# Optimization experiments

Measured on AMD Instinct MI355X. Metric: run time of the kernel, lower is better.

The kernel has to match this reference:

```python
import jax, jax.numpy as jnp
import numpy as np

B = 65536
H = W = 28
K = 3
OUT_HW = H - K + 1  # 26, valid conv
FEAT = OUT_HW * OUT_HW  # 676
HID = 200
NCLS = 10


def setup_inputs() -> dict:
    key = jax.random.key(0)
    ks = jax.random.split(key, 6)
    x = jax.random.normal(ks[0], (B, H * W), dtype=jnp.float32)
    conv_w = jnp.ones((K, K), dtype=jnp.float32)  # Parameter(ones((3,3)))
    w1 = jax.random.normal(ks[1], (FEAT, HID), dtype=jnp.float32) * (1.0 / np.sqrt(FEAT))
    b1 = jnp.zeros((HID,), dtype=jnp.float32)
    w2 = jax.random.normal(ks[2], (HID, NCLS), dtype=jnp.float32) * (1.0 / np.sqrt(HID))
    b2 = jnp.zeros((NCLS,), dtype=jnp.float32)
    return {"x": x, "conv_w": conv_w, "w1": w1, "b1": b1, "w2": w2, "b2": b2}


def _forward(x, conv_w, w1, b1, w2, b2):
    img = x.reshape(-1, H, W)  # (B,28,28)
    # valid 3x3 single-channel cross-correlation (matches input[i:i+3,j:j+3]*w)
    lhs = img[:, None, :, :]          # (B,1,28,28)
    rhs = conv_w[None, None, :, :]    # (1,1,3,3)
    conv = jax.lax.conv_general_dilated(
        lhs, rhs, window_strides=(1, 1), padding="VALID",
        dimension_numbers=("NCHW", "OIHW", "NCHW"))  # (B,1,26,26)
    feat = conv.reshape(-1, FEAT)     # (B,676)
    hidden = jax.nn.relu(feat @ w1 + b1)  # (B,200)
    return hidden @ w2 + b2               # (B,10) logits


def reference(x, conv_w, w1, b1, w2, b2):
    return _forward(x, conv_w, w1, b1, w2, b2)
```

## Files before the change

kernel.cpp:

```cpp
#include <hip/hip_runtime.h>
#include <hip/hip_bf16.h>

#define BATCH   65536
#define HW      28
#define OHW     26
#define FEAT    676
#define HID     200
#define NCLS    10
#define MT2     64
#define GBLOCKS (BATCH / MT2)
#define KC1     25

typedef __attribute__((ext_vector_type(8))) __bf16 bf16x8;
typedef __attribute__((ext_vector_type(4))) float  f32x4;

#define KBAR() asm volatile("s_waitcnt lgkmcnt(0)\n\ts_barrier" ::: "memory")

__device__ __forceinline__ unsigned int pk2(float a, float b) {
  __hip_bfloat16 ha = __float2bfloat16(a), hb = __float2bfloat16(b);
  return (unsigned int)__builtin_bit_cast(unsigned short, ha)
       | ((unsigned int)__builtin_bit_cast(unsigned short, hb) << 16);
}

__device__ __forceinline__ unsigned short* fslot(unsigned short* base, int m, int k) {
  const int kc = k >> 5;
  return base + ((kc * 64 + ((k >> 3) & 3) * 16 + (m ^ (kc & 7))) * 8) + (k & 7);
}

__global__ __launch_bounds__(256) void prep_w1e(const float* __restrict__ w1,
                                                const float* __restrict__ cwp,
                                                unsigned short* __restrict__ w1e) {
  int c = blockIdx.x * 256 + threadIdx.x;
  if (c >= KC1 * 13 * 64) return;
  int lane = c & 63, g = c >> 6;
  int kc = g / 13, nt = g - kc * 13;
  int ln = lane & 15, qd = lane >> 4;
  int n = nt * 16 + ln;
  float cw[9];
  #pragma unroll
  for (int t = 0; t < 9; ++t) cw[t] = cwp[t];
  float v[8];
  #pragma unroll
  for (int j = 0; j < 8; ++j) {
    int k = kc * 32 + qd * 8 + j;
    float s = 0.f;
    if (k < 784 && n < HID) {
      int ri = k / 28, ci = k - ri * 28;
      #pragma unroll
      for (int di = 0; di < 3; ++di) {
        int r = ri - di;
        if (r >= 0 && r < OHW) {
          #pragma unroll
          for (int dj = 0; dj < 3; ++dj) {
            int cc = ci - dj;
            if (cc >= 0 && cc < OHW) s += cw[di * 3 + dj] * w1[(r * OHW + cc) * HID + n];
          }
        }
      }
    }
    v[j] = s;
  }
  uint4 o = make_uint4(pk2(v[0], v[1]), pk2(v[2], v[3]),
                       pk2(v[4], v[5]), pk2(v[6], v[7]));
  *(uint4*)(w1e + (size_t)c * 8) = o;
}

__global__ __launch_bounds__(256) void prep_w2f(const float* __restrict__ w2,
                                                unsigned short* __restrict__ w2f) {
  int c = blockIdx.x * 256 + threadIdx.x;
  if (c >= 7 * 64) return;
  int lane = c & 63, kc = c >> 6;
  int col = lane & 15;
  float v[8];
  #pragma unroll
  for (int j = 0; j < 8; ++j) {
    int k = kc * 32 + (lane >> 4) * 8 + j;
    v[j] = (col < NCLS && k < HID) ? w2[k * NCLS + col] : 0.f;
  }
  uint4 o = make_uint4(pk2(v[0], v[1]), pk2(v[2], v[3]),
                       pk2(v[4], v[5]), pk2(v[6], v[7]));
  *(uint4*)(w2f + (size_t)c * 8) = o;
}

template<int NT0, int NT>
__device__ __forceinline__ void gemm1_body(
    const float* __restrict__ x, const unsigned short* __restrict__ w1e,
    const float* __restrict__ b1, unsigned short* aBuf ,
    unsigned short* hidA, int lane, int tid, int blk64) {
  const int ln = lane & 15, qd = lane >> 4;

  const int sc_mi  = tid >> 6;
  const int sc_qd  = (tid >> 4) & 3;
  const int sc_row = tid & 15;
  const float* xrow = x + ((size_t)blk64 + sc_mi * 16 + sc_row) * 784 + sc_qd * 8;
  const int sc_off = (sc_mi * 64 + sc_qd * 16 + sc_row) * 8;

  f32x4 acc[4][NT];
  #pragma unroll
  for (int mi = 0; mi < 4; ++mi)
    #pragma unroll
    for (int t = 0; t < NT; ++t) acc[mi][t] = (f32x4){0.f, 0.f, 0.f, 0.f};

  {
    float4 f0 = *(const float4*)(xrow);
    float4 f1 = *(const float4*)(xrow + 4);
    *(uint4*)(aBuf + sc_off) = make_uint4(pk2(f0.x, f0.y), pk2(f0.z, f0.w),
                                          pk2(f1.x, f1.y), pk2(f1.z, f1.w));
  }
  __syncthreads();

  int cur = 0;
  for (int kc = 0; kc < KC1; ++kc) {
    uint4 nx;
    const bool hav = (kc + 1 < KC1);
    if (hav) {
      if (kc + 1 == KC1 - 1 && sc_qd >= 2) {
        nx = make_uint4(0u, 0u, 0u, 0u);
      } else {
        float4 f0 = *(const float4*)(xrow + (kc + 1) * 32);
        float4 f1 = *(const float4*)(xrow + (kc + 1) * 32 + 4);
        nx = make_uint4(pk2(f0.x, f0.y), pk2(f0.z, f0.w),
                        pk2(f1.x, f1.y), pk2(f1.z, f1.w));
      }
    }
    const unsigned short* ab = aBuf + cur * 2048;
    bf16x8 a[4];
    #pragma unroll
    for (int mi = 0; mi < 4; ++mi)
      a[mi] = *(const bf16x8*)(ab + mi * 512 + lane * 8);
    #pragma unroll
    for (int t = 0; t < NT; ++t) {
      bf16x8 b = *(const bf16x8*)(w1e + ((size_t)(kc * 13 + NT0 + t) * 64 + lane) * 8);
      #pragma unroll
      for (int mi = 0; mi < 4; ++mi)
        acc[mi][t] = __builtin_amdgcn_mfma_f32_16x16x32_bf16(a[mi], b, acc[mi][t], 0, 0, 0);
    }
    if (hav) *(uint4*)(aBuf + (cur ^ 1) * 2048 + sc_off) = nx;
    KBAR();
    cur ^= 1;
  }

  #pragma unroll
  for (int t = 0; t < NT; ++t) {
    const int n = (NT0 + t) * 16 + ln;
    if (n < HID) {
      const float bias = b1[n];
      const int kc2 = n >> 5, qd2 = (n >> 3) & 3, j2 = n & 7, c2 = kc2 & 7;
      #pragma unroll
      for (int mi = 0; mi < 4; ++mi)
        #pragma unroll
        for (int rr = 0; rr < 4; ++rr) {
          const int m = qd * 4 + rr;
          float h = fmaxf(acc[mi][t][rr] + bias, 0.f);
          __hip_bfloat16 hb = __float2bfloat16(h);
          hidA[mi * 3584 + (kc2 * 64 + qd2 * 16 + (m ^ c2)) * 8 + j2] =
              __builtin_bit_cast(unsigned short, hb);
        }
    }
  }
}

__global__ __launch_bounds__(256, 4) void fused6(
    const float* __restrict__ x, const unsigned short* __restrict__ w1e,
    const unsigned short* __restrict__ w2f, const float* __restrict__ b1,
    const float* __restrict__ b2, float* __restrict__ out) {
  __shared__ __align__(16) unsigned short aBuf[2 * 4 * 64 * 8];
  __shared__ __align__(16) unsigned short hidA[4 * 7 * 64 * 8];
  const int tid  = threadIdx.x;
  const int wave = tid >> 6;
  const int lane = tid & 63;
  const int blk64 = blockIdx.x * MT2;

  for (int i = tid; i < 768; i += 256) {
    int mi = i / 192, r = i - mi * 192, m = r / 12, d = r - m * 12;
    *(unsigned int*)fslot(hidA + mi * 3584, m, 200 + 2 * d) = 0u;
  }

  switch (wave) {
    case 0:  gemm1_body<0, 4>(x, w1e, b1, aBuf, hidA, lane, tid, blk64); break;
    case 1:  gemm1_body<4, 3>(x, w1e, b1, aBuf, hidA, lane, tid, blk64); break;
    case 2:  gemm1_body<7, 3>(x, w1e, b1, aBuf, hidA, lane, tid, blk64); break;
    default: gemm1_body<10, 3>(x, w1e, b1, aBuf, hidA, lane, tid, blk64); break;
  }
  __syncthreads();

  const int ln = lane & 15, qd = lane >> 4;
  f32x4 acc2 = (f32x4){0.f, 0.f, 0.f, 0.f};
  #pragma unroll
  for (int kc = 0; kc < 7; ++kc) {
    bf16x8 a = *(const bf16x8*)&hidA[wave * 3584 + (kc * 64 + (lane ^ (kc & 7))) * 8];
    bf16x8 b = *(const bf16x8*)(w2f + ((size_t)kc * 64 + lane) * 8);
    acc2 = __builtin_amdgcn_mfma_f32_16x16x32_bf16(a, b, acc2, 0, 0, 0);
  }
  if (ln < NCLS) {
    const float bb = b2[ln];
    #pragma unroll
    for (int rr = 0; rr < 4; ++rr) {
      out[((size_t)(blockIdx.x * 4 + wave) * 16 + qd * 4 + rr) * NCLS + ln] = acc2[rr] + bb;
    }
  }
}

extern "C" void kernel_launch(void* const* d_in, const int* in_sizes, int n_in,
                              void* d_out, int out_size, void* d_ws, size_t ws_size,
                              hipStream_t stream) {
  const float* x  = (const float*)d_in[0];
  const float* cw = (const float*)d_in[1];
  const float* w1 = (const float*)d_in[2];
  const float* b1 = (const float*)d_in[3];
  const float* w2 = (const float*)d_in[4];
  const float* b2 = (const float*)d_in[5];
  float* out = (float*)d_out;

  unsigned short* w1e = (unsigned short*)d_ws;
  unsigned short* w2f = (unsigned short*)((char*)d_ws + 335872);

  hipLaunchKernelGGL(prep_w1e, dim3((KC1 * 13 * 64 + 255) / 256), dim3(256), 0, stream,
                     w1, cw, w1e);
  hipLaunchKernelGGL(prep_w2f, dim3(2), dim3(256), 0, stream, w2, w2f);
  hipLaunchKernelGGL(fused6, dim3(GBLOCKS), dim3(256), 0, stream,
                     x, w1e, w2f, b1, b2, out);
}
```

Baseline: 320.9 us.

## Stage W1 tiles through LDS with double buffering and triple-buffer the x tiles

Each block now cooperatively loads the per-k-chunk W1 fragments into a double-buffered LDS region instead of having each wave read them from global memory on every use. The x activation tiles move to a triple buffer so loads run two chunks ahead, and the hidden-activation buffer reuses the same shared region after the GEMM1 loop. The aim is to cut redundant global/L2 traffic for weights and hide load latency. In exchange each thread holds more in-flight registers and the block uses more LDS (about 38 KB), which could limit occupancy.

```diff
diff --git a/kernel.cpp b/kernel.cpp
--- a/kernel.cpp
+++ b/kernel.cpp
@@ -10,6 +10,11 @@
 #define MT2     64
 #define GBLOCKS (BATCH / MT2)
 #define KC1     25
+
+#define ABUF    2048
+#define BOFF    6144
+#define BBUF    6656
+#define SHTOT   19456
 
 typedef __attribute__((ext_vector_type(8))) __bf16 bf16x8;
 typedef __attribute__((ext_vector_type(4))) float  f32x4;
@@ -85,15 +90,13 @@
 template<int NT0, int NT>
 __device__ __forceinline__ void gemm1_body(
     const float* __restrict__ x, const unsigned short* __restrict__ w1e,
-    const float* __restrict__ b1, unsigned short* aBuf ,
-    unsigned short* hidA, int lane, int tid, int blk64) {
+    const float* __restrict__ b1, unsigned short* sh,
+    int lane, int tid, int blk64) {
   const int ln = lane & 15, qd = lane >> 4;
 
-  const int sc_mi  = tid >> 6;
-  const int sc_qd  = (tid >> 4) & 3;
-  const int sc_row = tid & 15;
-  const float* xrow = x + ((size_t)blk64 + sc_mi * 16 + sc_row) * 784 + sc_qd * 8;
-  const int sc_off = (sc_mi * 64 + sc_qd * 16 + sc_row) * 8;
+  const int sc_qd = (tid >> 4) & 3;
+  const float* xrow = x + ((size_t)blk64 + (tid >> 6) * 16 + (tid & 15)) * 784 + sc_qd * 8;
+  const int t3ok = (tid + 768) < 832;
 
   f32x4 acc[4][NT];
   #pragma unroll
@@ -104,40 +107,79 @@
   {
     float4 f0 = *(const float4*)(xrow);
     float4 f1 = *(const float4*)(xrow + 4);
-    *(uint4*)(aBuf + sc_off) = make_uint4(pk2(f0.x, f0.y), pk2(f0.z, f0.w),
-                                          pk2(f1.x, f1.y), pk2(f1.z, f1.w));
+    float4 g0 = *(const float4*)(xrow + 32);
+    float4 g1 = *(const float4*)(xrow + 36);
+    *(uint4*)(sh + tid * 8) = make_uint4(pk2(f0.x, f0.y), pk2(f0.z, f0.w),
+                                         pk2(f1.x, f1.y), pk2(f1.z, f1.w));
+    *(uint4*)(sh + ABUF + tid * 8) = make_uint4(pk2(g0.x, g0.y), pk2(g0.z, g0.w),
+                                                pk2(g1.x, g1.y), pk2(g1.z, g1.w));
+    uint4 b0 = *(const uint4*)(w1e + (size_t)tid * 8);
+    uint4 b1v = *(const uint4*)(w1e + (size_t)(tid + 256) * 8);
+    uint4 b2v = *(const uint4*)(w1e + (size_t)(tid + 512) * 8);
+    *(uint4*)(sh + BOFF + tid * 8) = b0;
+    *(uint4*)(sh + BOFF + (tid + 256) * 8) = b1v;
+    *(uint4*)(sh + BOFF + (tid + 512) * 8) = b2v;
+    if (t3ok) {
+      uint4 b3v = *(const uint4*)(w1e + (size_t)(tid + 768) * 8);
+      *(uint4*)(sh + BOFF + (tid + 768) * 8) = b3v;
+    }
   }
   __syncthreads();
 
-  int cur = 0;
   for (int kc = 0; kc < KC1; ++kc) {
-    uint4 nx;
-    const bool hav = (kc + 1 < KC1);
-    if (hav) {
-      if (kc + 1 == KC1 - 1 && sc_qd >= 2) {
-        nx = make_uint4(0u, 0u, 0u, 0u);
-      } else {
-        float4 f0 = *(const float4*)(xrow + (kc + 1) * 32);
-        float4 f1 = *(const float4*)(xrow + (kc + 1) * 32 + 4);
-        nx = make_uint4(pk2(f0.x, f0.y), pk2(f0.z, f0.w),
-                        pk2(f1.x, f1.y), pk2(f1.z, f1.w));
-      }
-    }
-    const unsigned short* ab = aBuf + cur * 2048;
+    uint4 bq0, bq1, bq2, bq3;
+    const bool havB = (kc + 1 < KC1);
+    if (havB) {
+      const unsigned short* wsrc = w1e + (size_t)(kc + 1) * 832 * 8;
+      bq0 = *(const uint4*)(wsrc + (size_t)tid * 8);
+      bq1 = *(const uint4*)(wsrc + (size_t)(tid + 256) * 8);
+      bq2 = *(const uint4*)(wsrc + (size_t)(tid + 512) * 8);
+      if (t3ok) bq3 = *(const uint4*)(wsrc + (size_t)(tid + 768) * 8);
+    }
+    float4 fq0, fq1;
+    const bool havA = (kc + 2 < KC1);
+    const bool atail = (kc + 2 == KC1 - 1) && (sc_qd >= 2);
+    if (havA && !atail) {
+      fq0 = *(const float4*)(xrow + (kc + 2) * 32);
+      fq1 = *(const float4*)(xrow + (kc + 2) * 32 + 4);
+    }
+
+    const unsigned short* ab = sh + (kc % 3) * ABUF;
+    const unsigned short* bb = sh + BOFF + (kc & 1) * BBUF;
     bf16x8 a[4];
     #pragma unroll
     for (int mi = 0; mi < 4; ++mi)
       a[mi] = *(const bf16x8*)(ab + mi * 512 + lane * 8);
     #pragma unroll
     for (int t = 0; t < NT; ++t) {
-      bf16x8 b = *(const bf16x8*)(w1e + ((size_t)(kc * 13 + NT0 + t) * 64 + lane) * 8);
+      bf16x8 b = *(const bf16x8*)(bb + ((NT0 + t) * 64 + lane) * 8);
       #pragma unroll
       for (int mi = 0; mi < 4; ++mi)
         acc[mi][t] = __builtin_amdgcn_mfma_f32_16x16x32_bf16(a[mi], b, acc[mi][t], 0, 0, 0);
     }
-    if (hav) *(uint4*)(aBuf + (cur ^ 1) * 2048 + sc_off) = nx;
+
+    if (havA) {
+      uint4 cv;
+      if (atail) cv = make_uint4(0u, 0u, 0u, 0u);
+      else       cv = make_uint4(pk2(fq0.x, fq0.y), pk2(fq0.z, fq0.w),
+                                 pk2(fq1.x, fq1.y), pk2(fq1.z, fq1.w));
+      *(uint4*)(sh + ((kc + 2) % 3) * ABUF + tid * 8) = cv;
+    }
+    if (havB) {
+      unsigned short* bdst = sh + BOFF + ((kc + 1) & 1) * BBUF;
+      *(uint4*)(bdst + tid * 8) = bq0;
+      *(uint4*)(bdst + (tid + 256) * 8) = bq1;
+      *(uint4*)(bdst + (tid + 512) * 8) = bq2;
+      if (t3ok) *(uint4*)(bdst + (tid + 768) * 8) = bq3;
+    }
     KBAR();
-    cur ^= 1;
+  }
+
+  __syncthreads();
+
+  for (int i = tid; i < 768; i += 256) {
+    int mi = i / 192, r = i - mi * 192, m = r / 12, d = r - m * 12;
+    *(unsigned int*)fslot(sh + mi * 3584, m, 200 + 2 * d) = 0u;
   }
 
   #pragma unroll
@@ -153,34 +195,28 @@
           const int m = qd * 4 + rr;
           float h = fmaxf(acc[mi][t][rr] + bias, 0.f);
           __hip_bfloat16 hb = __float2bfloat16(h);
-          hidA[mi * 3584 + (kc2 * 64 + qd2 * 16 + (m ^ c2)) * 8 + j2] =
+          sh[mi * 3584 + (kc2 * 64 + qd2 * 16 + (m ^ c2)) * 8 + j2] =
               __builtin_bit_cast(unsigned short, hb);
         }
     }
   }
 }
 
-__global__ __launch_bounds__(256, 4) void fused6(
+__global__ __launch_bounds__(256, 4) void fused7(
     const float* __restrict__ x, const unsigned short* __restrict__ w1e,
     const unsigned short* __restrict__ w2f, const float* __restrict__ b1,
     const float* __restrict__ b2, float* __restrict__ out) {
-  __shared__ __align__(16) unsigned short aBuf[2 * 4 * 64 * 8];
-  __shared__ __align__(16) unsigned short hidA[4 * 7 * 64 * 8];
+  __shared__ __align__(16) unsigned short sh[SHTOT];
   const int tid  = threadIdx.x;
   const int wave = tid >> 6;
   const int lane = tid & 63;
   const int blk64 = blockIdx.x * MT2;
 
-  for (int i = tid; i < 768; i += 256) {
-    int mi = i / 192, r = i - mi * 192, m = r / 12, d = r - m * 12;
-    *(unsigned int*)fslot(hidA + mi * 3584, m, 200 + 2 * d) = 0u;
-  }
-
   switch (wave) {
-    case 0:  gemm1_body<0, 4>(x, w1e, b1, aBuf, hidA, lane, tid, blk64); break;
-    case 1:  gemm1_body<4, 3>(x, w1e, b1, aBuf, hidA, lane, tid, blk64); break;
-    case 2:  gemm1_body<7, 3>(x, w1e, b1, aBuf, hidA, lane, tid, blk64); break;
-    default: gemm1_body<10, 3>(x, w1e, b1, aBuf, hidA, lane, tid, blk64); break;
+    case 0:  gemm1_body<0, 4>(x, w1e, b1, sh, lane, tid, blk64); break;
+    case 1:  gemm1_body<4, 3>(x, w1e, b1, sh, lane, tid, blk64); break;
+    case 2:  gemm1_body<7, 3>(x, w1e, b1, sh, lane, tid, blk64); break;
+    default: gemm1_body<10, 3>(x, w1e, b1, sh, lane, tid, blk64); break;
   }
   __syncthreads();
 
@@ -188,7 +224,7 @@
   f32x4 acc2 = (f32x4){0.f, 0.f, 0.f, 0.f};
   #pragma unroll
   for (int kc = 0; kc < 7; ++kc) {
-    bf16x8 a = *(const bf16x8*)&hidA[wave * 3584 + (kc * 64 + (lane ^ (kc & 7))) * 8];
+    bf16x8 a = *(const bf16x8*)&sh[wave * 3584 + (kc * 64 + (lane ^ (kc & 7))) * 8];
     bf16x8 b = *(const bf16x8*)(w2f + ((size_t)kc * 64 + lane) * 8);
     acc2 = __builtin_amdgcn_mfma_f32_16x16x32_bf16(a, b, acc2, 0, 0, 0);
   }
@@ -218,6 +254,6 @@
   hipLaunchKernelGGL(prep_w1e, dim3((KC1 * 13 * 64 + 255) / 256), dim3(256), 0, stream,
                      w1, cw, w1e);
   hipLaunchKernelGGL(prep_w2f, dim3(2), dim3(256), 0, stream, w2, w2f);
-  hipLaunchKernelGGL(fused6, dim3(GBLOCKS), dim3(256), 0, stream,
+  hipLaunchKernelGGL(fused7, dim3(GBLOCKS), dim3(256), 0, stream,
                      x, w1e, w2f, b1, b2, out);
 }
```

New measurement: 323.6 us. No clear change (+0.8%).

## Deepen x prefetch to distance two and register-prefetch W1 fragments

Applied to the files above, without the earlier changes.

The GEMM1 K-loop now loads x rows two chunks ahead into registers and also prefetches the next chunk's W1 B-fragments into registers, so global loads overlap with the MFMAs instead of being issued just before use. The loop is fully unrolled and the staging offset is simplified to tid*8. Launch bounds drop from 4 to 3 blocks per CU to make room for the extra registers. The cost is higher register pressure and lower occupancy.

```diff
diff --git a/kernel.cpp b/kernel.cpp
--- a/kernel.cpp
+++ b/kernel.cpp
@@ -20,6 +20,11 @@
   __hip_bfloat16 ha = __float2bfloat16(a), hb = __float2bfloat16(b);
   return (unsigned int)__builtin_bit_cast(unsigned short, ha)
        | ((unsigned int)__builtin_bit_cast(unsigned short, hb) << 16);
+}
+
+__device__ __forceinline__ uint4 pk8(float4 f0, float4 f1) {
+  return make_uint4(pk2(f0.x, f0.y), pk2(f0.z, f0.w),
+                    pk2(f1.x, f1.y), pk2(f1.z, f1.w));
 }
 
 __device__ __forceinline__ unsigned short* fslot(unsigned short* base, int m, int k) {
@@ -89,11 +94,9 @@
     unsigned short* hidA, int lane, int tid, int blk64) {
   const int ln = lane & 15, qd = lane >> 4;
 
-  const int sc_mi  = tid >> 6;
-  const int sc_qd  = (tid >> 4) & 3;
-  const int sc_row = tid & 15;
-  const float* xrow = x + ((size_t)blk64 + sc_mi * 16 + sc_row) * 784 + sc_qd * 8;
-  const int sc_off = (sc_mi * 64 + sc_qd * 16 + sc_row) * 8;
+  const int sc_qd = (tid >> 4) & 3;
+  const float* xrow =
+      x + ((size_t)blk64 + (tid >> 6) * 16 + (tid & 15)) * 784 + sc_qd * 8;
 
   f32x4 acc[4][NT];
   #pragma unroll
@@ -102,42 +105,57 @@
     for (int t = 0; t < NT; ++t) acc[mi][t] = (f32x4){0.f, 0.f, 0.f, 0.f};
 
   {
-    float4 f0 = *(const float4*)(xrow);
-    float4 f1 = *(const float4*)(xrow + 4);
-    *(uint4*)(aBuf + sc_off) = make_uint4(pk2(f0.x, f0.y), pk2(f0.z, f0.w),
-                                          pk2(f1.x, f1.y), pk2(f1.z, f1.w));
-  }
+    float4 p0 = *(const float4*)(xrow);
+    float4 p1 = *(const float4*)(xrow + 4);
+    *(uint4*)(aBuf + tid * 8) = pk8(p0, p1);
+  }
+  float4 a1l0 = *(const float4*)(xrow + 32), a1l1 = *(const float4*)(xrow + 36);
+  float4 a2l0 = *(const float4*)(xrow + 64), a2l1 = *(const float4*)(xrow + 68);
+  bf16x8 bCur[NT];
+  #pragma unroll
+  for (int t = 0; t < NT; ++t)
+    bCur[t] = *(const bf16x8*)(w1e + ((size_t)((NT0 + t) * 64 + lane)) * 8);
   __syncthreads();
 
-  int cur = 0;
+  #pragma unroll
   for (int kc = 0; kc < KC1; ++kc) {
-    uint4 nx;
-    const bool hav = (kc + 1 < KC1);
-    if (hav) {
-      if (kc + 1 == KC1 - 1 && sc_qd >= 2) {
-        nx = make_uint4(0u, 0u, 0u, 0u);
+    if (kc + 1 < KC1)
+      *(uint4*)(aBuf + ((kc + 1) & 1) * 2048 + tid * 8) = pk8(a1l0, a1l1);
+    a1l0 = a2l0; a1l1 = a2l1;
+
+    bf16x8 bNx[NT];
+    if (kc + 1 < KC1) {
+      #pragma unroll
+      for (int t = 0; t < NT; ++t)
+        bNx[t] = *(const bf16x8*)(w1e +
+                   ((size_t)((kc + 1) * 13 + NT0 + t) * 64 + lane) * 8);
+    }
+    if (kc + 3 < KC1) {
+      if (kc + 3 == KC1 - 1 && sc_qd >= 2) {
+        a2l0 = (float4){0.f, 0.f, 0.f, 0.f};
+        a2l1 = (float4){0.f, 0.f, 0.f, 0.f};
       } else {
-        float4 f0 = *(const float4*)(xrow + (kc + 1) * 32);
-        float4 f1 = *(const float4*)(xrow + (kc + 1) * 32 + 4);
-        nx = make_uint4(pk2(f0.x, f0.y), pk2(f0.z, f0.w),
-                        pk2(f1.x, f1.y), pk2(f1.z, f1.w));
+        a2l0 = *(const float4*)(xrow + (kc + 3) * 32);
+        a2l1 = *(const float4*)(xrow + (kc + 3) * 32 + 4);
       }
     }
-    const unsigned short* ab = aBuf + cur * 2048;
+
+    const unsigned short* ab = aBuf + (kc & 1) * 2048;
     bf16x8 a[4];
     #pragma unroll
     for (int mi = 0; mi < 4; ++mi)
       a[mi] = *(const bf16x8*)(ab + mi * 512 + lane * 8);
     #pragma unroll
-    for (int t = 0; t < NT; ++t) {
-      bf16x8 b = *(const bf16x8*)(w1e + ((size_t)(kc * 13 + NT0 + t) * 64 + lane) * 8);
+    for (int t = 0; t < NT; ++t)
       #pragma unroll
       for (int mi = 0; mi < 4; ++mi)
-        acc[mi][t] = __builtin_amdgcn_mfma_f32_16x16x32_bf16(a[mi], b, acc[mi][t], 0, 0, 0);
-    }
-    if (hav) *(uint4*)(aBuf + (cur ^ 1) * 2048 + sc_off) = nx;
+        acc[mi][t] = __builtin_amdgcn_mfma_f32_16x16x32_bf16(a[mi], bCur[t],
+                                                             acc[mi][t], 0, 0, 0);
+    if (kc + 1 < KC1) {
+      #pragma unroll
+      for (int t = 0; t < NT; ++t) bCur[t] = bNx[t];
+    }
     KBAR();
-    cur ^= 1;
   }
 
   #pragma unroll
@@ -160,11 +178,11 @@
   }
 }
 
-__global__ __launch_bounds__(256, 4) void fused6(
+__global__ __launch_bounds__(256, 3) void fused8(
     const float* __restrict__ x, const unsigned short* __restrict__ w1e,
     const unsigned short* __restrict__ w2f, const float* __restrict__ b1,
     const float* __restrict__ b2, float* __restrict__ out) {
-  __shared__ __align__(16) unsigned short aBuf[2 * 4 * 64 * 8];
+  __shared__ __align__(16) unsigned short aBuf[2 * 2048];
   __shared__ __align__(16) unsigned short hidA[4 * 7 * 64 * 8];
   const int tid  = threadIdx.x;
   const int wave = tid >> 6;
@@ -218,6 +236,6 @@
   hipLaunchKernelGGL(prep_w1e, dim3((KC1 * 13 * 64 + 255) / 256), dim3(256), 0, stream,
                      w1, cw, w1e);
   hipLaunchKernelGGL(prep_w2f, dim3(2), dim3(256), 0, stream, w2, w2f);
-  hipLaunchKernelGGL(fused6, dim3(GBLOCKS), dim3(256), 0, stream,
+  hipLaunchKernelGGL(fused8, dim3(GBLOCKS), dim3(256), 0, stream,
                      x, w1e, w2f, b1, b2, out);
 }
```

Measured after the change: 328.0 us. 1.02x slower.

## Process two K-chunks per barrier, share LDS for hidden, merge prep kernels

Applied to the files above, without the earlier changes.

The GEMM1 loop now stages 64 K-elements per iteration (two 32-wide chunks) into a double buffer, halving the number of barriers and making each prefetch larger. The staging buffer and hidden-activation buffer are merged into one shared array, with the epilogue moved after a barrier, which reduces LDS per block and may help occupancy. The two weight-prep kernels are merged into one launch. The loop is fully unrolled, which raises register pressure and can cost spills.

```diff
diff --git a/kernel.cpp b/kernel.cpp
--- a/kernel.cpp
+++ b/kernel.cpp
@@ -4,12 +4,12 @@
 #define BATCH   65536
 #define HW      28
 #define OHW     26
-#define FEAT    676
 #define HID     200
 #define NCLS    10
 #define MT2     64
 #define GBLOCKS (BATCH / MT2)
-#define KC1     25
+#define KC32    26
+#define NSTEP   13
 
 typedef __attribute__((ext_vector_type(8))) __bf16 bf16x8;
 typedef __attribute__((ext_vector_type(4))) float  f32x4;
@@ -22,124 +22,151 @@
        | ((unsigned int)__builtin_bit_cast(unsigned short, hb) << 16);
 }
 
+__device__ __forceinline__ uint4 pk8(float4 f0, float4 f1) {
+  return make_uint4(pk2(f0.x, f0.y), pk2(f0.z, f0.w),
+                    pk2(f1.x, f1.y), pk2(f1.z, f1.w));
+}
+
 __device__ __forceinline__ unsigned short* fslot(unsigned short* base, int m, int k) {
   const int kc = k >> 5;
   return base + ((kc * 64 + ((k >> 3) & 3) * 16 + (m ^ (kc & 7))) * 8) + (k & 7);
 }
 
-__global__ __launch_bounds__(256) void prep_w1e(const float* __restrict__ w1,
-                                                const float* __restrict__ cwp,
-                                                unsigned short* __restrict__ w1e) {
-  int c = blockIdx.x * 256 + threadIdx.x;
-  if (c >= KC1 * 13 * 64) return;
-  int lane = c & 63, g = c >> 6;
-  int kc = g / 13, nt = g - kc * 13;
-  int ln = lane & 15, qd = lane >> 4;
-  int n = nt * 16 + ln;
-  float cw[9];
-  #pragma unroll
-  for (int t = 0; t < 9; ++t) cw[t] = cwp[t];
-  float v[8];
-  #pragma unroll
-  for (int j = 0; j < 8; ++j) {
-    int k = kc * 32 + qd * 8 + j;
-    float s = 0.f;
-    if (k < 784 && n < HID) {
-      int ri = k / 28, ci = k - ri * 28;
-      #pragma unroll
-      for (int di = 0; di < 3; ++di) {
-        int r = ri - di;
-        if (r >= 0 && r < OHW) {
-          #pragma unroll
-          for (int dj = 0; dj < 3; ++dj) {
-            int cc = ci - dj;
-            if (cc >= 0 && cc < OHW) s += cw[di * 3 + dj] * w1[(r * OHW + cc) * HID + n];
+__global__ __launch_bounds__(256) void prep_weights(
+    const float* __restrict__ w1, const float* __restrict__ cwp,
+    const float* __restrict__ w2, unsigned short* __restrict__ w1e,
+    unsigned short* __restrict__ w2f) {
+  if (blockIdx.x < 85) {
+    int c = blockIdx.x * 256 + threadIdx.x;
+    if (c >= KC32 * 13 * 64) return;
+    int lane = c & 63, g = c >> 6;
+    int kc = g / 13, nt = g - kc * 13;
+    int ln = lane & 15, qd = lane >> 4;
+    int n = nt * 16 + ln;
+    float cw[9];
+    #pragma unroll
+    for (int t = 0; t < 9; ++t) cw[t] = cwp[t];
+    float v[8];
+    #pragma unroll
+    for (int j = 0; j < 8; ++j) {
+      int k = kc * 32 + qd * 8 + j;
+      float s = 0.f;
+      if (k < 784 && n < HID) {
+        int ri = k / 28, ci = k - ri * 28;
+        #pragma unroll
+        for (int di = 0; di < 3; ++di) {
+          int r = ri - di;
+          if (r >= 0 && r < OHW) {
+            #pragma unroll
+            for (int dj = 0; dj < 3; ++dj) {
+              int cc = ci - dj;
+              if (cc >= 0 && cc < OHW)
+                s += cw[di * 3 + dj] * w1[(r * OHW + cc) * HID + n];
+            }
           }
         }
       }
-    }
-    v[j] = s;
-  }
-  uint4 o = make_uint4(pk2(v[0], v[1]), pk2(v[2], v[3]),
-                       pk2(v[4], v[5]), pk2(v[6], v[7]));
-  *(uint4*)(w1e + (size_t)c * 8) = o;
-}
-
-__global__ __launch_bounds__(256) void prep_w2f(const float* __restrict__ w2,
-                                                unsigned short* __restrict__ w2f) {
-  int c = blockIdx.x * 256 + threadIdx.x;
-  if (c >= 7 * 64) return;
-  int lane = c & 63, kc = c >> 6;
-  int col = lane & 15;
-  float v[8];
-  #pragma unroll
-  for (int j = 0; j < 8; ++j) {
-    int k = kc * 32 + (lane >> 4) * 8 + j;
-    v[j] = (col < NCLS && k < HID) ? w2[k * NCLS + col] : 0.f;
-  }
-  uint4 o = make_uint4(pk2(v[0], v[1]), pk2(v[2], v[3]),
-                       pk2(v[4], v[5]), pk2(v[6], v[7]));
-  *(uint4*)(w2f + (size_t)c * 8) = o;
+      v[j] = s;
+    }
+    *(uint4*)(w1e + (size_t)c * 8) =
+        make_uint4(pk2(v[0], v[1]), pk2(v[2], v[3]),
+                   pk2(v[4], v[5]), pk2(v[6], v[7]));
+  } else {
+    int c = (blockIdx.x - 85) * 256 + threadIdx.x;
+    if (c >= 7 * 64) return;
+    int lane = c & 63, kc = c >> 6;
+    int col = lane & 15;
+    float v[8];
+    #pragma unroll
+    for (int j = 0; j < 8; ++j) {
+      int k = kc * 32 + (lane >> 4) * 8 + j;
+      v[j] = (col < NCLS && k < HID) ? w2[k * NCLS + col] : 0.f;
+    }
+    *(uint4*)(w2f + (size_t)c * 8) =
+        make_uint4(pk2(v[0], v[1]), pk2(v[2], v[3]),
+                   pk2(v[4], v[5]), pk2(v[6], v[7]));
+  }
 }
 
 template<int NT0, int NT>
-__device__ __forceinline__ void gemm1_body(
+__device__ __forceinline__ void gemm1_compute(
     const float* __restrict__ x, const unsigned short* __restrict__ w1e,
-    const float* __restrict__ b1, unsigned short* aBuf ,
-    unsigned short* hidA, int lane, int tid, int blk64) {
-  const int ln = lane & 15, qd = lane >> 4;
-
-  const int sc_mi  = tid >> 6;
-  const int sc_qd  = (tid >> 4) & 3;
-  const int sc_row = tid & 15;
-  const float* xrow = x + ((size_t)blk64 + sc_mi * 16 + sc_row) * 784 + sc_qd * 8;
-  const int sc_off = (sc_mi * 64 + sc_qd * 16 + sc_row) * 8;
-
-  f32x4 acc[4][NT];
-  #pragma unroll
-  for (int mi = 0; mi < 4; ++mi)
-    #pragma unroll
-    for (int t = 0; t < NT; ++t) acc[mi][t] = (f32x4){0.f, 0.f, 0.f, 0.f};
+    unsigned short* sh, int lane, int tid, int blk64, f32x4 (&acc)[4][4]) {
+  const int sc_qd = (tid >> 4) & 3;
+  const float* xrow =
+      x + ((size_t)blk64 + (tid >> 6) * 16 + (tid & 15)) * 784;
+  const int koff = sc_qd * 8;
+  const int soff = tid * 8;
 
   {
-    float4 f0 = *(const float4*)(xrow);
-    float4 f1 = *(const float4*)(xrow + 4);
-    *(uint4*)(aBuf + sc_off) = make_uint4(pk2(f0.x, f0.y), pk2(f0.z, f0.w),
-                                          pk2(f1.x, f1.y), pk2(f1.z, f1.w));
+    float4 f0 = *(const float4*)(xrow + koff);
+    float4 f1 = *(const float4*)(xrow + koff + 4);
+    float4 g0 = *(const float4*)(xrow + 32 + koff);
+    float4 g1 = *(const float4*)(xrow + 32 + koff + 4);
+    *(uint4*)(sh + soff)        = pk8(f0, f1);
+    *(uint4*)(sh + 2048 + soff) = pk8(g0, g1);
   }
   __syncthreads();
 
   int cur = 0;
-  for (int kc = 0; kc < KC1; ++kc) {
-    uint4 nx;
-    const bool hav = (kc + 1 < KC1);
+  #pragma unroll
+  for (int s = 0; s < NSTEP; ++s) {
+    float4 p00, p01, p10, p11;
+    const bool hav = (s + 1 < NSTEP);
     if (hav) {
-      if (kc + 1 == KC1 - 1 && sc_qd >= 2) {
-        nx = make_uint4(0u, 0u, 0u, 0u);
+      const int kb = (s + 1) * 64;
+      if (s + 1 == NSTEP - 1) {
+        if (sc_qd < 2) {
+          p00 = *(const float4*)(xrow + 768 + koff);
+          p01 = *(const float4*)(xrow + 768 + koff + 4);
+        } else {
+          p00 = (float4){0.f, 0.f, 0.f, 0.f};
+          p01 = (float4){0.f, 0.f, 0.f, 0.f};
+        }
+        p10 = (float4){0.f, 0.f, 0.f, 0.f};
+        p11 = (float4){0.f, 0.f, 0.f, 0.f};
       } else {
-        float4 f0 = *(const float4*)(xrow + (kc + 1) * 32);
-        float4 f1 = *(const float4*)(xrow + (kc + 1) * 32 + 4);
-        nx = make_uint4(pk2(f0.x, f0.y), pk2(f0.z, f0.w),
-                        pk2(f1.x, f1.y), pk2(f1.z, f1.w));
+        p00 = *(const float4*)(xrow + kb + koff);
+        p01 = *(const float4*)(xrow + kb + koff + 4);
+        p10 = *(const float4*)(xrow + kb + 32 + koff);
+        p11 = *(const float4*)(xrow + kb + 32 + koff + 4);
       }
     }
-    const unsigned short* ab = aBuf + cur * 2048;
-    bf16x8 a[4];
-    #pragma unroll
-    for (int mi = 0; mi < 4; ++mi)
-      a[mi] = *(const bf16x8*)(ab + mi * 512 + lane * 8);
-    #pragma unroll
-    for (int t = 0; t < NT; ++t) {
-      bf16x8 b = *(const bf16x8*)(w1e + ((size_t)(kc * 13 + NT0 + t) * 64 + lane) * 8);
+
+    const unsigned short* ab = sh + cur * 4096;
+    #pragma unroll
+    for (int h = 0; h < 2; ++h) {
+      bf16x8 a[4];
       #pragma unroll
       for (int mi = 0; mi < 4; ++mi)
-        acc[mi][t] = __builtin_amdgcn_mfma_f32_16x16x32_bf16(a[mi], b, acc[mi][t], 0, 0, 0);
-    }
-    if (hav) *(uint4*)(aBuf + (cur ^ 1) * 2048 + sc_off) = nx;
+        a[mi] = *(const bf16x8*)(ab + h * 2048 + mi * 512 + lane * 8);
+      const int kc32 = s * 2 + h;
+      #pragma unroll
+      for (int t = 0; t < NT; ++t) {
+        bf16x8 b = *(const bf16x8*)(w1e +
+                     ((size_t)(kc32 * 13 + NT0 + t) * 64 + lane) * 8);
+        #pragma unroll
+        for (int mi = 0; mi < 4; ++mi)
+          acc[mi][t] = __builtin_amdgcn_mfma_f32_16x16x32_bf16(a[mi], b,
+                                                               acc[mi][t], 0, 0, 0);
+      }
+    }
+
+    if (hav) {
+      unsigned short* dst = sh + (cur ^ 1) * 4096;
+      *(uint4*)(dst + soff)        = pk8(p00, p01);
+      *(uint4*)(dst + 2048 + soff) = pk8(p10, p11);
+    }
     KBAR();
     cur ^= 1;
   }
-
+}
+
+template<int NT0, int NT>
+__device__ __forceinline__ void gemm1_epilogue(
+    const float* __restrict__ b1, unsigned short* hidA, int lane,
+    f32x4 (&acc)[4][4]) {
+  const int ln = lane & 15, qd = lane >> 4;
   #pragma unroll
   for (int t = 0; t < NT; ++t) {
     const int n = (NT0 + t) * 16 + ln;
@@ -160,27 +187,39 @@
   }
 }
 
-__global__ __launch_bounds__(256, 4) void fused6(
+__global__ __launch_bounds__(256, 4) void fused10(
     const float* __restrict__ x, const unsigned short* __restrict__ w1e,
     const unsigned short* __restrict__ w2f, const float* __restrict__ b1,
     const float* __restrict__ b2, float* __restrict__ out) {
-  __shared__ __align__(16) unsigned short aBuf[2 * 4 * 64 * 8];
-  __shared__ __align__(16) unsigned short hidA[4 * 7 * 64 * 8];
+  __shared__ __align__(16) unsigned short sh[4 * 3584];
   const int tid  = threadIdx.x;
   const int wave = tid >> 6;
   const int lane = tid & 63;
   const int blk64 = blockIdx.x * MT2;
 
+  f32x4 acc[4][4];
+  #pragma unroll
+  for (int mi = 0; mi < 4; ++mi)
+    #pragma unroll
+    for (int t = 0; t < 4; ++t) acc[mi][t] = (f32x4){0.f, 0.f, 0.f, 0.f};
+
+  switch (wave) {
+    case 0:  gemm1_compute<0, 4>(x, w1e, sh, lane, tid, blk64, acc); break;
+    case 1:  gemm1_compute<4, 3>(x, w1e, sh, lane, tid, blk64, acc); break;
+    case 2:  gemm1_compute<7, 3>(x, w1e, sh, lane, tid, blk64, acc); break;
+    default: gemm1_compute<10, 3>(x, w1e, sh, lane, tid, blk64, acc); break;
+  }
+  __syncthreads();
+
   for (int i = tid; i < 768; i += 256) {
     int mi = i / 192, r = i - mi * 192, m = r / 12, d = r - m * 12;
-    *(unsigned int*)fslot(hidA + mi * 3584, m, 200 + 2 * d) = 0u;
-  }
-
+    *(unsigned int*)fslot(sh + mi * 3584, m, 200 + 2 * d) = 0u;
+  }
   switch (wave) {
-    case 0:  gemm1_body<0, 4>(x, w1e, b1, aBuf, hidA, lane, tid, blk64); break;
-    case 1:  gemm1_body<4, 3>(x, w1e, b1, aBuf, hidA, lane, tid, blk64); break;
-    case 2:  gemm1_body<7, 3>(x, w1e, b1, aBuf, hidA, lane, tid, blk64); break;
-    default: gemm1_body<10, 3>(x, w1e, b1, aBuf, hidA, lane, tid, blk64); break;
+    case 0:  gemm1_epilogue<0, 4>(b1, sh, lane, acc); break;
+    case 1:  gemm1_epilogue<4, 3>(b1, sh, lane, acc); break;
+    case 2:  gemm1_epilogue<7, 3>(b1, sh, lane, acc); break;
+    default: gemm1_epilogue<10, 3>(b1, sh, lane, acc); break;
   }
   __syncthreads();
 
@@ -188,7 +227,7 @@
   f32x4 acc2 = (f32x4){0.f, 0.f, 0.f, 0.f};
   #pragma unroll
   for (int kc = 0; kc < 7; ++kc) {
-    bf16x8 a = *(const bf16x8*)&hidA[wave * 3584 + (kc * 64 + (lane ^ (kc & 7))) * 8];
+    bf16x8 a = *(const bf16x8*)&sh[wave * 3584 + (kc * 64 + (lane ^ (kc & 7))) * 8];
     bf16x8 b = *(const bf16x8*)(w2f + ((size_t)kc * 64 + lane) * 8);
     acc2 = __builtin_amdgcn_mfma_f32_16x16x32_bf16(a, b, acc2, 0, 0, 0);
   }
@@ -196,7 +235,8 @@
     const float bb = b2[ln];
     #pragma unroll
     for (int rr = 0; rr < 4; ++rr) {
-      out[((size_t)(blockIdx.x * 4 + wave) * 16 + qd * 4 + rr) * NCLS + ln] = acc2[rr] + bb;
+      out[((size_t)(blockIdx.x * 4 + wave) * 16 + qd * 4 + rr) * NCLS + ln] =
+          acc2[rr] + bb;
     }
   }
 }
@@ -213,11 +253,10 @@
   float* out = (float*)d_out;
 
   unsigned short* w1e = (unsigned short*)d_ws;
-  unsigned short* w2f = (unsigned short*)((char*)d_ws + 335872);
-
-  hipLaunchKernelGGL(prep_w1e, dim3((KC1 * 13 * 64 + 255) / 256), dim3(256), 0, stream,
-                     w1, cw, w1e);
-  hipLaunchKernelGGL(prep_w2f, dim3(2), dim3(256), 0, stream, w2, w2f);
-  hipLaunchKernelGGL(fused6, dim3(GBLOCKS), dim3(256), 0, stream,
+  unsigned short* w2f = (unsigned short*)((char*)d_ws + 348160);
+
+  hipLaunchKernelGGL(prep_weights, dim3(87), dim3(256), 0, stream,
+                     w1, cw, w2, w1e, w2f);
+  hipLaunchKernelGGL(fused10, dim3(GBLOCKS), dim3(256), 0, stream,
                      x, w1e, w2f, b1, b2, out);
 }
```

Measured after the change: 325.6 us. About the same (+1.5%).
